# Optimization experiments

Measured on AMD Instinct MI355X. Metric: run time of the kernel, lower is better.

The kernel has to match this reference:

```python
import jax, jax.numpy as jnp
import numpy as np

B, L, XS, YS, A, C, NL = 32, 4096, 256, 256, 4, 64, 5  # batch, seq, x_size, y_size, n_actions, hid_cnn, cnn_layers


def _conv2d(x, w):
    # x: [N,Cin,H,W], w: [Cout,Cin,3,3], stride 1, pad 1 ('SAME')
    return jax.lax.conv_general_dilated(x, w, (1, 1), 'SAME',
                                        dimension_numbers=('NCHW', 'OIHW', 'NCHW'))


def setup_inputs() -> dict:
    key = jax.random.key(0)
    ks = jax.random.split(key, 16)
    stdv = 1.0 / np.sqrt(XS)
    inp = {
        'x': jax.random.normal(ks[0], (B, L, XS), jnp.float32),
        'y': jax.random.normal(ks[1], (B, YS), jnp.float32),
        'x_mask': jax.random.randint(ks[2], (B, L), 0, 2) == 1,
        'actions': jax.random.randint(ks[3], (B,), 0, A),
        'weight': jax.random.uniform(ks[4], (YS, XS), jnp.float32, -stdv, stdv),
    }
    chans = [(1, C)] + [(C, C)] * (NL - 2) + [(C, 1)]
    for i, (ci, co) in enumerate(chans):
        bound = 1.0 / np.sqrt(ci * 9)
        inp[f'cw{i}'] = jax.random.uniform(ks[5 + 2 * i], (A, co, ci, 3, 3), jnp.float32, -bound, bound)
        inp[f'cb{i}'] = jax.random.uniform(ks[6 + 2 * i], (A, co), jnp.float32, -bound, bound)
    return inp


def reference(x, y, x_mask, actions, weight,
              cw0, cb0, cw1, cb1, cw2, cb2, cw3, cb3, cw4, cb4):
    img = weight[None, None]  # [1,1,YS,XS] -- weight matrix as a 1-channel image

    def per_action(w0, b0, w1, b1, w2, b2, w3, b3, w4, b4):
        out = img
        layers = ((w0, b0), (w1, b1), (w2, b2), (w3, b3), (w4, b4))
        for i, (w, b) in enumerate(layers):
            out = _conv2d(out, w) + b[None, :, None, None]
            if i < NL - 1:
                out = jax.nn.relu(out)
        return out[0, 0]  # [YS,XS]

    # all per-action conv stacks batched via vmap -> [A,YS,XS]
    W_a = jax.vmap(per_action)(cw0, cb0, cw1, cb1, cw2, cb2, cw3, cb3, cw4, cb4)
    # one-hot multiply + sum over actions == select the per-sample action matrix
    Wy = jnp.einsum('bh,bhx->bx', y, W_a[actions])          # [B,XS]
    xWy = jnp.einsum('blx,bx->bl', x, Wy)                   # [B,L]
    xWy = jnp.where(x_mask, -jnp.inf, xWy)
    return jax.nn.softmax(xWy, axis=-1)  # eval-mode output (training uses log_softmax)
```

## Files before the change

kernel.cpp:

```cpp
#include <hip/hip_runtime.h>
#include <cstdint>
#include <cstddef>

typedef __attribute__((ext_vector_type(8))) short bf16x8;
typedef __attribute__((ext_vector_type(4))) float f32x4;
typedef __attribute__((ext_vector_type(4))) int i32x4;

__device__ inline unsigned short cvt_bf16_rne(float f) {
    unsigned u = __builtin_bit_cast(unsigned, f);
    u = (u + 0x7FFFu + ((u >> 16) & 1u)) >> 16;
    return (unsigned short)u;
}
__device__ inline float bf16_to_f32(unsigned short s) {
    return __builtin_bit_cast(float, (unsigned)s << 16);
}

__global__ void detect_mask_kernel(const unsigned int* m, int* flag) {
    int i = blockIdx.x * blockDim.x + threadIdx.x;
    int f = 0;
    #pragma unroll
    for (int k = 0; k < 4; ++k) {
        unsigned int v = m[i * 4 + k];
        if (v == 0x3F800000u) f |= 2;
        else if (v > 1u) f |= 1;
    }
    if (f) atomicOr(flag, f);
}

__global__ void apack_all_kernel(const float* __restrict__ cw1,
                                 const float* __restrict__ cw2,
                                 const float* __restrict__ cw3,
                                 char* __restrict__ apack,
                                 int* __restrict__ flag) {
    int t = threadIdx.x;
    int tap = blockIdx.x, a = blockIdx.y, lz = blockIdx.z;
    if (tap == 0 && a == 0 && lz == 0 && t == 0) *flag = 0;
    const float* cw = (lz == 0) ? cw1 : (lz == 1 ? cw2 : cw3);
    char* outp = apack + (size_t)lz * 294912;
    int ks = t >> 8, mf = (t >> 6) & 3, lane = t & 63;
    int n = lane & 15, q = lane >> 4;
    int co = mf * 16 + n;
    int ci0 = ks * 32 + q * 8;
    unsigned d[4];
    #pragma unroll
    for (int jj = 0; jj < 4; ++jj) {
        unsigned short h0 = cvt_bf16_rne(cw[((size_t)(a * 64 + co) * 64 + ci0 + 2 * jj + 0) * 9 + tap]);
        unsigned short h1 = cvt_bf16_rne(cw[((size_t)(a * 64 + co) * 64 + ci0 + 2 * jj + 1) * 9 + tap]);
        d[jj] = (unsigned)h0 | ((unsigned)h1 << 16);
    }
    *(i32x4*)(outp + ((((size_t)(a * 9 + tap) * 2 + ks) * 4 + mf) * 1024 + lane * 16)) =
        *(i32x4*)d;
}

__device__ __forceinline__ void conv_mid_body(const i32x4* lds4,
                                              const char* __restrict__ apack_l,
                                              const float* __restrict__ cb,
                                              unsigned short* __restrict__ act_out,
                                              int a, int r0, int c0, int tid) {
    int lane = tid & 63, wv = tid >> 6;
    int n = lane & 15, q = lane >> 4;

    f32x4 acc[4][4];
    #pragma unroll
    for (int mf = 0; mf < 4; ++mf) {
        f32x4 bb = *(const f32x4*)(cb + a * 64 + mf * 16 + q * 4);
        #pragma unroll
        for (int nf = 0; nf < 4; ++nf) acc[mf][nf] = bb;
    }

    int base_nf[4];
    #pragma unroll
    for (int nf = 0; nf < 4; ++nf) {
        int orl = wv * 2 + (nf >> 1);
        int ocl = ((nf & 1) << 4) + n;
        base_nf[nf] = (orl * 34 + ocl) * 9 + q;
    }
    const char* ap = apack_l + (size_t)a * 9 * 8192 + lane * 16;

    #pragma unroll
    for (int tap = 0; tap < 9; ++tap) {
        const int ty = tap / 3, tx = tap - ty * 3;
        const int toff = (ty * 34 + tx) * 9;
        #pragma unroll
        for (int ks = 0; ks < 2; ++ks) {
            bf16x8 Af[4], Bf[4];
            #pragma unroll
            for (int mf = 0; mf < 4; ++mf)
                Af[mf] = __builtin_bit_cast(bf16x8,
                    *(const i32x4*)(ap + (((tap * 2 + ks) * 4 + mf) << 10)));
            #pragma unroll
            for (int nf = 0; nf < 4; ++nf)
                Bf[nf] = __builtin_bit_cast(bf16x8, lds4[base_nf[nf] + toff + ks * 4]);
            #pragma unroll
            for (int mf = 0; mf < 4; ++mf)
                #pragma unroll
                for (int nf = 0; nf < 4; ++nf)
                    acc[mf][nf] = __builtin_amdgcn_mfma_f32_16x16x32_bf16(
                        Af[mf], Bf[nf], acc[mf][nf], 0, 0, 0);
        }
    }

    #pragma unroll
    for (int nf = 0; nf < 4; ++nf) {
        int grow = r0 + wv * 2 + (nf >> 1);
        int gcol = c0 + ((nf & 1) << 4) + n;
        char* ob = (char*)act_out + (((size_t)(a << 16) + (grow << 8) + gcol) << 7) + q * 8;
        #pragma unroll
        for (int mf = 0; mf < 4; ++mf) {
            f32x4 v = acc[mf][nf];
            unsigned d0 = (unsigned)cvt_bf16_rne(fmaxf(v.x, 0.0f))
                        | ((unsigned)cvt_bf16_rne(fmaxf(v.y, 0.0f)) << 16);
            unsigned d1 = (unsigned)cvt_bf16_rne(fmaxf(v.z, 0.0f))
                        | ((unsigned)cvt_bf16_rne(fmaxf(v.w, 0.0f)) << 16);
            uint2 st; st.x = d0; st.y = d1;
            *(uint2*)(ob + mf * 32) = st;
        }
    }
}

__global__ __launch_bounds__(256, 3)
void conv_mid_mfma(const unsigned short* __restrict__ act_in,
                   const char* __restrict__ apack_l,
                   const float* __restrict__ cb,
                   unsigned short* __restrict__ act_out) {
    __shared__ i32x4 lds4[340 * 9];
    int tid = threadIdx.x;
    int a = blockIdx.z;
    int r0 = blockIdx.y * 8, c0 = blockIdx.x * 32;
    const char* actb = (const char*)act_in;

    for (int s = tid; s < 2720; s += 256) {
        int px = s >> 3, o = s & 7;
        int prow = px / 34, pcol = px - prow * 34;
        int grow = r0 - 1 + prow, gcol = c0 - 1 + pcol;
        i32x4 v = {0, 0, 0, 0};
        if ((unsigned)grow < 256u && (unsigned)gcol < 256u)
            v = *(const i32x4*)(actb + (((size_t)(a << 16) + (grow << 8) + gcol) << 7) + (o << 4));
        lds4[px * 9 + o] = v;
    }
    __syncthreads();
    conv_mid_body(lds4, apack_l, cb, act_out, a, r0, c0, tid);
}

__global__ __launch_bounds__(256, 3)
void conv_mid_fused0(const float* __restrict__ img,
                     const float* __restrict__ cw0,
                     const float* __restrict__ cb0,
                     const char* __restrict__ apack_l,
                     const float* __restrict__ cb,
                     unsigned short* __restrict__ act_out) {
    __shared__ i32x4 lds4[340 * 9];
    __shared__ float img_s[12 * 36];
    int tid = threadIdx.x;
    int a = blockIdx.z;
    int r0 = blockIdx.y * 8, c0 = blockIdx.x * 32;

    for (int s = tid; s < 432; s += 256) {
        int ir = s / 36, ic = s - ir * 36;
        int gr = r0 - 2 + ir, gc = c0 - 2 + ic;
        img_s[s] = ((unsigned)gr < 256u && (unsigned)gc < 256u) ? img[gr * 256 + gc] : 0.0f;
    }
    __syncthreads();

    int o = tid & 7;
    float wr[8][9], br[8];
    #pragma unroll
    for (int j = 0; j < 8; ++j) {
        const float* wp = cw0 + ((size_t)a * 64 + o * 8 + j) * 9;
        #pragma unroll
        for (int t = 0; t < 9; ++t) wr[j][t] = wp[t];
        br[j] = cb0[a * 64 + o * 8 + j];
    }

    for (int s = tid; s < 2720; s += 256) {
        int px = s >> 3;
        int prow = px / 34, pcol = px - prow * 34;
        int grow = r0 - 1 + prow, gcol = c0 - 1 + pcol;
        i32x4 v = {0, 0, 0, 0};
        if ((unsigned)grow < 256u && (unsigned)gcol < 256u) {
            float accv[8];
            #pragma unroll
            for (int j = 0; j < 8; ++j) accv[j] = br[j];
            #pragma unroll
            for (int dy = 0; dy < 3; ++dy)
                #pragma unroll
                for (int dx = 0; dx < 3; ++dx) {
                    float iv = img_s[(prow + dy) * 36 + (pcol + dx)];
                    #pragma unroll
                    for (int j = 0; j < 8; ++j)
                        accv[j] = fmaf(wr[j][dy * 3 + dx], iv, accv[j]);
                }
            unsigned d[4];
            #pragma unroll
            for (int jj = 0; jj < 4; ++jj) {
                unsigned short h0 = cvt_bf16_rne(fmaxf(accv[2 * jj + 0], 0.0f));
                unsigned short h1 = cvt_bf16_rne(fmaxf(accv[2 * jj + 1], 0.0f));
                d[jj] = (unsigned)h0 | ((unsigned)h1 << 16);
            }
            v = *(i32x4*)d;
        }
        lds4[px * 9 + o] = v;
    }
    __syncthreads();
    conv_mid_body(lds4, apack_l, cb, act_out, a, r0, c0, tid);
}

__global__ void conv_last_kernel(const unsigned short* __restrict__ act,
                                 const float* __restrict__ cw4,
                                 const float* __restrict__ cb4,
                                 float* __restrict__ W_a) {
    int y = blockIdx.x, a = blockIdx.y;
    int tid = threadIdx.x;
    int lane = tid & 63, wv = tid >> 6;
    int o = lane & 7, pl = lane >> 3;
    float wr[8][9];
    #pragma unroll
    for (int j = 0; j < 8; ++j) {
        const float* wp = cw4 + ((size_t)a * 64 + o * 8 + j) * 9;
        #pragma unroll
        for (int t = 0; t < 9; ++t) wr[j][t] = wp[t];
    }
    const char* actb = (const char*)act;
    float bias = cb4[a];
    for (int i = 0; i < 8; ++i) {
        int x = i * 32 + wv * 8 + pl;
        float p = 0.0f;
        #pragma unroll
        for (int ty = 0; ty < 3; ++ty) {
            int py = y + ty - 1;
            #pragma unroll
            for (int tx = 0; tx < 3; ++tx) {
                int px = x + tx - 1;
                if ((unsigned)py < 256u && (unsigned)px < 256u) {
                    i32x4 v = *(const i32x4*)(actb +
                        (((size_t)(a << 16) + (py << 8) + px) << 7) + (o << 4));
                    const unsigned* dv = (const unsigned*)&v;
                    #pragma unroll
                    for (int j = 0; j < 8; ++j) {
                        unsigned d = dv[j >> 1];
                        unsigned short us = (j & 1) ? (unsigned short)(d >> 16)
                                                    : (unsigned short)(d & 0xffffu);
                        p = fmaf(bf16_to_f32(us), wr[j][ty * 3 + tx], p);
                    }
                }
            }
        }
        p += __shfl_xor(p, 1, 64);
        p += __shfl_xor(p, 2, 64);
        p += __shfl_xor(p, 4, 64);
        if (o == 0) W_a[(size_t)(a << 16) + (y << 8) + x] = p + bias;
    }
}

__global__ void wy_kernel(const float* __restrict__ yv,
                          const int* __restrict__ actions,
                          const float* __restrict__ W_a,
                          float* __restrict__ Wy) {
    int b = blockIdx.x, x = threadIdx.x;
    int a = actions[b];
    const float* Wp = W_a + (size_t)a * 65536;
    const float* yb = yv + b * 256;
    float acc = 0.0f;
    #pragma unroll 8
    for (int h = 0; h < 256; ++h)
        acc = fmaf(yb[h], Wp[(size_t)h * 256 + x], acc);
    Wy[b * 256 + x] = acc;
}

__global__ void logits_kernel(const float* __restrict__ xv,
                              const void* __restrict__ mask,
                              const int* __restrict__ flag,
                              const float* __restrict__ Wy,
                              float* __restrict__ out) {
    int tid = threadIdx.x, lane = tid & 63, wave = tid >> 6;
    int b = blockIdx.y;
    int fl = *flag;
    float4 wy4 = *(const float4*)(Wy + b * 256 + lane * 4);
    const float* xb = xv + (size_t)b * 4096 * 256;
    int l0 = blockIdx.x * 128 + wave * 32;
    float ninf = -__builtin_inff();
    for (int li = 0; li < 32; li += 4) {
        int l = l0 + li;
        const float* rp = xb + (size_t)l * 256 + lane * 4;
        float4 x0 = *(const float4*)(rp);
        float4 x1 = *(const float4*)(rp + 256);
        float4 x2 = *(const float4*)(rp + 512);
        float4 x3 = *(const float4*)(rp + 768);
        float p0 = x0.x * wy4.x + x0.y * wy4.y + x0.z * wy4.z + x0.w * wy4.w;
        float p1 = x1.x * wy4.x + x1.y * wy4.y + x1.z * wy4.z + x1.w * wy4.w;
        float p2 = x2.x * wy4.x + x2.y * wy4.y + x2.z * wy4.z + x2.w * wy4.w;
        float p3 = x3.x * wy4.x + x3.y * wy4.y + x3.z * wy4.z + x3.w * wy4.w;
        #pragma unroll
        for (int off = 32; off > 0; off >>= 1) {
            p0 += __shfl_xor(p0, off, 64);
            p1 += __shfl_xor(p1, off, 64);
            p2 += __shfl_xor(p2, off, 64);
            p3 += __shfl_xor(p3, off, 64);
        }
        if (lane == 0) {
            size_t mi = (size_t)b * 4096 + l;
            float4 r;
            r.x = p0; r.y = p1; r.z = p2; r.w = p3;
            if (fl & 2) {
                const float* mp = (const float*)mask + mi;
                if (mp[0] != 0.0f) r.x = ninf;
                if (mp[1] != 0.0f) r.y = ninf;
                if (mp[2] != 0.0f) r.z = ninf;
                if (mp[3] != 0.0f) r.w = ninf;
            } else if (fl & 1) {
                const unsigned char* mp = (const unsigned char*)mask + mi;
                if (mp[0]) r.x = ninf;
                if (mp[1]) r.y = ninf;
                if (mp[2]) r.z = ninf;
                if (mp[3]) r.w = ninf;
            } else {
                const int* mp = (const int*)mask + mi;
                if (mp[0]) r.x = ninf;
                if (mp[1]) r.y = ninf;
                if (mp[2]) r.z = ninf;
                if (mp[3]) r.w = ninf;
            }
            *(float4*)(out + mi) = r;
        }
    }
}

__global__ void softmax_kernel(float* __restrict__ out) {
    int b = blockIdx.x, tid = threadIdx.x;
    int lane = tid & 63, wid = tid >> 6;
    float* row = out + (size_t)b * 4096;
    float v[4];
    float m = -__builtin_inff();
    #pragma unroll
    for (int i = 0; i < 4; ++i) { v[i] = row[tid + i * 1024]; m = fmaxf(m, v[i]); }
    #pragma unroll
    for (int off = 32; off > 0; off >>= 1) m = fmaxf(m, __shfl_xor(m, off, 64));
    __shared__ float redm[16];
    __shared__ float reds[16];
    if (lane == 0) redm[wid] = m;
    __syncthreads();
    float M = redm[0];
    #pragma unroll
    for (int j = 1; j < 16; ++j) M = fmaxf(M, redm[j]);
    float s = 0.0f;
    #pragma unroll
    for (int i = 0; i < 4; ++i) { v[i] = expf(v[i] - M); s += v[i]; }
    #pragma unroll
    for (int off = 32; off > 0; off >>= 1) s += __shfl_xor(s, off, 64);
    if (lane == 0) reds[wid] = s;
    __syncthreads();
    float S = 0.0f;
    #pragma unroll
    for (int j = 0; j < 16; ++j) S += reds[j];
    float inv = 1.0f / S;
    #pragma unroll
    for (int i = 0; i < 4; ++i) row[tid + i * 1024] = v[i] * inv;
}

extern "C" void kernel_launch(void* const* d_in, const int* in_sizes, int n_in,
                              void* d_out, int out_size, void* d_ws, size_t ws_size,
                              hipStream_t stream) {
    const float* xv      = (const float*)d_in[0];
    const float* yv      = (const float*)d_in[1];
    const void*  xmask   = d_in[2];
    const int*   actions = (const int*)d_in[3];
    const float* weight  = (const float*)d_in[4];
    const float* cw0 = (const float*)d_in[5];
    const float* cb0 = (const float*)d_in[6];
    const float* cw1 = (const float*)d_in[7];
    const float* cb1 = (const float*)d_in[8];
    const float* cw2 = (const float*)d_in[9];
    const float* cb2 = (const float*)d_in[10];
    const float* cw3 = (const float*)d_in[11];
    const float* cb3 = (const float*)d_in[12];
    const float* cw4 = (const float*)d_in[13];
    const float* cb4 = (const float*)d_in[14];
    float* out = (float*)d_out;

    char* ws = (char*)d_ws;
    unsigned short* bufA = (unsigned short*)ws;
    unsigned short* bufB = (unsigned short*)(ws + 33554432);
    char*  apack = ws + 67108864;
    float* W_a   = (float*)(ws + 67993600);
    float* Wy    = (float*)(ws + 69042176);
    int*   flag  = (int*)(ws + 69074944);

    apack_all_kernel<<<dim3(9, 4, 3), 512, 0, stream>>>(cw1, cw2, cw3, apack, flag);
    detect_mask_kernel<<<32, 256, 0, stream>>>((const unsigned int*)xmask, flag);

    conv_mid_fused0<<<dim3(8, 32, 4), 256, 0, stream>>>(weight, cw0, cb0, apack, cb1, bufA);
    conv_mid_mfma<<<dim3(8, 32, 4), 256, 0, stream>>>(bufA, apack + 294912, cb2, bufB);
    conv_mid_mfma<<<dim3(8, 32, 4), 256, 0, stream>>>(bufB, apack + 589824, cb3, bufA);
    conv_last_kernel<<<dim3(256, 4), 256, 0, stream>>>(bufA, cw4, cb4, W_a);

    wy_kernel<<<32, 256, 0, stream>>>(yv, actions, W_a, Wy);
    logits_kernel<<<dim3(32, 32), 256, 0, stream>>>(xv, xmask, flag, Wy, out);
    softmax_kernel<<<32, 1024, 0, stream>>>(out);
}
```

Before: 362.9 us.

## Split wy reduction across lanes and restructure logits reduction via shared memory

The wy kernel now splits each output column's 256-term reduction across 4 threads (1024 threads per block) and combines the partial sums with shuffles. The logits kernel drops the per-row full wave butterfly reduction. Each lane keeps a partial dot product, does a single xor-16 shuffle, and writes it to shared memory, then each lane sums one row's partials and writes one output with a per-row mask lookup. This cuts shuffle count and lane-0-only serial stores, at the cost of LDS traffic, a barrier per pass, and a quarter as many blocks (8x32 grid).

```diff
diff --git a/kernel.cpp b/kernel.cpp
--- a/kernel.cpp
+++ b/kernel.cpp
@@ -256,15 +256,20 @@
                           const int* __restrict__ actions,
                           const float* __restrict__ W_a,
                           float* __restrict__ Wy) {
-    int b = blockIdx.x, x = threadIdx.x;
+    int b = blockIdx.x, t = threadIdx.x;
+    int x = t >> 2, hq = t & 3;
     int a = actions[b];
     const float* Wp = W_a + (size_t)a * 65536;
     const float* yb = yv + b * 256;
     float acc = 0.0f;
     #pragma unroll 8
-    for (int h = 0; h < 256; ++h)
+    for (int i = 0; i < 64; ++i) {
+        int h = i * 4 + hq;
         acc = fmaf(yb[h], Wp[(size_t)h * 256 + x], acc);
-    Wy[b * 256 + x] = acc;
+    }
+    acc += __shfl_xor(acc, 1, 64);
+    acc += __shfl_xor(acc, 2, 64);
+    if (hq == 0) Wy[b * 256 + x] = acc;
 }
 
 __global__ void logits_kernel(const float* __restrict__ xv,
@@ -272,56 +277,40 @@
                               const int* __restrict__ flag,
                               const float* __restrict__ Wy,
                               float* __restrict__ out) {
-    int tid = threadIdx.x, lane = tid & 63, wave = tid >> 6;
+    __shared__ float part[4][64][36];
+    int tid = threadIdx.x, lane = tid & 63, w = tid >> 6;
     int b = blockIdx.y;
     int fl = *flag;
     float4 wy4 = *(const float4*)(Wy + b * 256 + lane * 4);
     const float* xb = xv + (size_t)b * 4096 * 256;
-    int l0 = blockIdx.x * 128 + wave * 32;
+    int slot = (lane & 15) | ((lane >> 5) << 4);
+    bool wr = (lane & 16) == 0;
     float ninf = -__builtin_inff();
-    for (int li = 0; li < 32; li += 4) {
-        int l = l0 + li;
-        const float* rp = xb + (size_t)l * 256 + lane * 4;
-        float4 x0 = *(const float4*)(rp);
-        float4 x1 = *(const float4*)(rp + 256);
-        float4 x2 = *(const float4*)(rp + 512);
-        float4 x3 = *(const float4*)(rp + 768);
-        float p0 = x0.x * wy4.x + x0.y * wy4.y + x0.z * wy4.z + x0.w * wy4.w;
-        float p1 = x1.x * wy4.x + x1.y * wy4.y + x1.z * wy4.z + x1.w * wy4.w;
-        float p2 = x2.x * wy4.x + x2.y * wy4.y + x2.z * wy4.z + x2.w * wy4.w;
-        float p3 = x3.x * wy4.x + x3.y * wy4.y + x3.z * wy4.z + x3.w * wy4.w;
-        #pragma unroll
-        for (int off = 32; off > 0; off >>= 1) {
-            p0 += __shfl_xor(p0, off, 64);
-            p1 += __shfl_xor(p1, off, 64);
-            p2 += __shfl_xor(p2, off, 64);
-            p3 += __shfl_xor(p3, off, 64);
-        }
-        if (lane == 0) {
-            size_t mi = (size_t)b * 4096 + l;
-            float4 r;
-            r.x = p0; r.y = p1; r.z = p2; r.w = p3;
-            if (fl & 2) {
-                const float* mp = (const float*)mask + mi;
-                if (mp[0] != 0.0f) r.x = ninf;
-                if (mp[1] != 0.0f) r.y = ninf;
-                if (mp[2] != 0.0f) r.z = ninf;
-                if (mp[3] != 0.0f) r.w = ninf;
-            } else if (fl & 1) {
-                const unsigned char* mp = (const unsigned char*)mask + mi;
-                if (mp[0]) r.x = ninf;
-                if (mp[1]) r.y = ninf;
-                if (mp[2]) r.z = ninf;
-                if (mp[3]) r.w = ninf;
-            } else {
-                const int* mp = (const int*)mask + mi;
-                if (mp[0]) r.x = ninf;
-                if (mp[1]) r.y = ninf;
-                if (mp[2]) r.z = ninf;
-                if (mp[3]) r.w = ninf;
-            }
-            *(float4*)(out + mi) = r;
-        }
+
+    #pragma unroll
+    for (int pass = 0; pass < 2; ++pass) {
+        int rowbase = blockIdx.x * 512 + pass * 256 + w * 64;
+        #pragma unroll 4
+        for (int li = 0; li < 64; ++li) {
+            const float4 x4 = *(const float4*)(xb + (size_t)(rowbase + li) * 256 + lane * 4);
+            float p = x4.x * wy4.x + x4.y * wy4.y + x4.z * wy4.z + x4.w * wy4.w;
+            p += __shfl_xor(p, 16, 64);
+            if (wr) part[w][li][slot] = p;
+        }
+        float s = 0.0f;
+        #pragma unroll
+        for (int j = 0; j < 8; ++j) {
+            f32x4 v4 = *(const f32x4*)&part[w][lane][j * 4];
+            s += (v4.x + v4.y) + (v4.z + v4.w);
+        }
+        int r = rowbase + lane;
+        size_t mi = (size_t)b * 4096 + r;
+        bool msk;
+        if (fl & 2)      msk = ((const float*)mask)[mi] != 0.0f;
+        else if (fl & 1) msk = ((const unsigned char*)mask)[mi] != 0;
+        else             msk = ((const int*)mask)[mi] != 0;
+        out[mi] = msk ? ninf : s;
+        __syncthreads();
     }
 }
 
@@ -393,7 +382,7 @@
     conv_mid_mfma<<<dim3(8, 32, 4), 256, 0, stream>>>(bufB, apack + 589824, cb3, bufA);
     conv_last_kernel<<<dim3(256, 4), 256, 0, stream>>>(bufA, cw4, cb4, W_a);
 
-    wy_kernel<<<32, 256, 0, stream>>>(yv, actions, W_a, Wy);
-    logits_kernel<<<dim3(32, 32), 256, 0, stream>>>(xv, xmask, flag, Wy, out);
+    wy_kernel<<<32, 1024, 0, stream>>>(yv, actions, W_a, Wy);
+    logits_kernel<<<dim3(8, 32), 256, 0, stream>>>(xv, xmask, flag, Wy, out);
     softmax_kernel<<<32, 1024, 0, stream>>>(out);
 }
```

Measured after the change: 401.4 us. 10.6% more time.
